# Kernel tuning notes

Measured on AMD Instinct MI355X. Metric: run time of the kernel, lower is better.

## Reference

```python
import jax, jax.numpy as jnp
import numpy as np

N = 100000      # n_nodes
E = 1600000     # n_edges (avg degree 16)
IN_C = 256
OUT_C = 64
HID = OUT_C * 2  # 128


def setup_inputs() -> dict:
    key = jax.random.key(0)
    k = jax.random.split(key, 4)
    x = jax.random.normal(k[0], (N, IN_C), dtype=jnp.float32)
    edge_index = jax.random.randint(k[1], (2, E), 0, N, dtype=jnp.int64)
    W1 = jax.random.normal(k[2], (IN_C, HID), dtype=jnp.float32) * (1.0 / np.sqrt(IN_C))
    b1 = jnp.zeros((HID,), dtype=jnp.float32)
    W2 = jax.random.normal(k[3], (HID, OUT_C), dtype=jnp.float32) * (1.0 / np.sqrt(HID))
    b2 = jnp.zeros((OUT_C,), dtype=jnp.float32)
    return {"x": x, "edge_index": edge_index, "W1": W1, "b1": b1, "W2": W2, "b2": b2}


def reference(x, edge_index, W1, b1, W2, b2):
    n = x.shape[0]
    # GCNConv default: add self-loops, symmetric normalization D^-1/2 A D^-1/2
    loop = jnp.arange(n, dtype=edge_index.dtype)
    src = jnp.concatenate([edge_index[0], loop])  # [E+N]
    dst = jnp.concatenate([edge_index[1], loop])  # [E+N]
    deg = jax.ops.segment_sum(jnp.ones_like(dst, dtype=x.dtype), dst, num_segments=n)
    dis = jax.lax.rsqrt(deg)  # deg >= 1 thanks to self-loops
    norm = dis[src] * dis[dst]  # [E+N]

    def gcn_conv(h, W, b):
        h = h @ W                                   # [n, d_out] dense transform first
        msg = h[src] * norm[:, None]                # [E+N, d_out] gather + scale
        return jax.ops.segment_sum(msg, dst, num_segments=n) + b

    h = jax.nn.relu(gcn_conv(x, W1, b1))
    return gcn_conv(h, W2, b2)
```

## Files before the change

### kernel.cpp

```cpp
#include <hip/hip_runtime.h>
#include <hip/hip_bf16.h>


#define GCN_IN_C 256
#define GCN_HID  128
#define GCN_OUT  64

#define BKT_SHIFT 8
#define BKT_NODES 256
#define EPB 4096

typedef __bf16 bf16x8 __attribute__((ext_vector_type(8)));
typedef __bf16 bf16x4 __attribute__((ext_vector_type(4)));
typedef float f32x4 __attribute__((ext_vector_type(4)));

__global__ __launch_bounds__(256) void k_bucket_hist(const int* __restrict__ dst,
                                                     int* __restrict__ bcnt, int e, int nb) {
  __shared__ int h[512];
  int tid = threadIdx.x;
  h[tid] = 0; h[tid + 256] = 0;
  __syncthreads();
  int base = blockIdx.x * EPB;
#pragma unroll
  for (int j = 0; j < EPB / 256; ++j) {
    int i = base + j * 256 + tid;
    if (i < e) atomicAdd(&h[dst[i] >> BKT_SHIFT], 1);
  }
  __syncthreads();
  if (tid < nb && h[tid]) atomicAdd(&bcnt[tid], h[tid]);
  if (tid + 256 < nb && h[tid + 256]) atomicAdd(&bcnt[tid + 256], h[tid + 256]);
}

__global__ __launch_bounds__(512) void k_scan_buckets(const int* __restrict__ bcnt,
                                                      int* __restrict__ bbase,
                                                      int* __restrict__ bcur, int nb) {
  __shared__ int sh[512];
  int t = threadIdx.x;
  int v = (t < nb) ? bcnt[t] : 0;
  sh[t] = v;
  __syncthreads();
  for (int d = 1; d < 512; d <<= 1) {
    int x = (t >= d) ? sh[t - d] : 0;
    __syncthreads();
    sh[t] += x;
    __syncthreads();
  }
  if (t < nb) {
    int ex = sh[t] - v;
    bbase[t] = ex;
    bcur[t] = ex;
  }
}

__global__ __launch_bounds__(256) void k_partition(const int* __restrict__ src,
                                                   const int* __restrict__ dst,
                                                   int* __restrict__ bcur,
                                                   unsigned int* __restrict__ part,
                                                   int e, int nb) {
  __shared__ int h[512];
  __shared__ int base[512];
  int tid = threadIdx.x;
  h[tid] = 0; h[tid + 256] = 0;
  __syncthreads();
  int b0 = blockIdx.x * EPB;
  int s[EPB / 256], d[EPB / 256], rk[EPB / 256];
#pragma unroll
  for (int j = 0; j < EPB / 256; ++j) {
    int i = b0 + j * 256 + tid;
    if (i < e) {
      s[j] = src[i];
      d[j] = dst[i];
      rk[j] = atomicAdd(&h[d[j] >> BKT_SHIFT], 1);
    }
  }
  __syncthreads();
  if (tid < nb && h[tid]) base[tid] = atomicAdd(&bcur[tid], h[tid]);
  if (tid + 256 < nb && h[tid + 256]) base[tid + 256] = atomicAdd(&bcur[tid + 256], h[tid + 256]);
  __syncthreads();
#pragma unroll
  for (int j = 0; j < EPB / 256; ++j) {
    int i = b0 + j * 256 + tid;
    if (i < e) {
      int bk = d[j] >> BKT_SHIFT;
      unsigned int dl = (unsigned int)(d[j] & (BKT_NODES - 1));
      part[base[bk] + rk[j]] = (dl << 24) | (unsigned int)s[j];
    }
  }
}

__global__ __launch_bounds__(256) void k_bucket_csr(
    const unsigned int* __restrict__ part, const int* __restrict__ bbase,
    const int* __restrict__ bcnt, int* __restrict__ off, int* __restrict__ end,
    float* __restrict__ dis, int* __restrict__ csr, int n) {
  __shared__ int cnt[256];
  __shared__ int sc[256];
  __shared__ int cur[256];
  int b = blockIdx.x, tid = threadIdx.x;
  int node0 = b << BKT_SHIFT;
  int eb0 = bbase[b];
  int ebn = bcnt[b];
  cnt[tid] = 0;
  __syncthreads();
  for (int i = tid; i < ebn; i += 256) atomicAdd(&cnt[part[eb0 + i] >> 24], 1);
  __syncthreads();
  int v = cnt[tid];
  sc[tid] = v;
  __syncthreads();
  for (int dd = 1; dd < 256; dd <<= 1) {
    int x = (tid >= dd) ? sc[tid - dd] : 0;
    __syncthreads();
    sc[tid] += x;
    __syncthreads();
  }
  int lo = sc[tid] - v;
  cur[tid] = lo;
  int node = node0 + tid;
  if (node < n) {
    off[node] = eb0 + lo;
    end[node] = eb0 + lo + v;
    dis[node] = rsqrtf((float)v + 1.0f);
  }
  __syncthreads();
  for (int i = tid; i < ebn; i += 256) {
    unsigned int u = part[eb0 + i];
    int r = atomicAdd(&cur[u >> 24], 1);
    csr[eb0 + r] = (int)(u & 0xFFFFFFu);
  }
}

template<int K, int NOUT>
__device__ __forceinline__ void split_w_one(const float* __restrict__ W,
                                            __bf16* __restrict__ Wsp, int idx) {
  int n = idx % NOUT;
  int g = (idx / NOUT) & 3;
  int ks = idx / (4 * NOUT);
  __bf16* hi = Wsp + (size_t)ks * (2 * 4 * NOUT * 8) + ((size_t)g * NOUT + n) * 8;
  __bf16* lo = hi + 4 * NOUT * 8;
#pragma unroll
  for (int j = 0; j < 8; ++j) {
    float f = W[(size_t)(ks * 32 + g * 8 + j) * NOUT + n];
    __bf16 h = (__bf16)f;
    hi[j] = h;
    lo[j] = (__bf16)(f - (float)h);
  }
}

__global__ __launch_bounds__(256) void k_split_w_all(
    const float* __restrict__ W1, __bf16* __restrict__ w1sp,
    const float* __restrict__ W2, __bf16* __restrict__ w2sp) {
  constexpr int N1 = (GCN_IN_C / 32) * 4 * GCN_HID;
  constexpr int N2 = (GCN_HID / 32) * 4 * GCN_OUT;
  int idx = blockIdx.x * 256 + threadIdx.x;
  if (idx < N1) split_w_one<GCN_IN_C, GCN_HID>(W1, w1sp, idx);
  else if (idx < N1 + N2) split_w_one<GCN_HID, GCN_OUT>(W2, w2sp, idx - N1);
}

template<int K, int NOUT>
__global__ __launch_bounds__(256, 5) void k_gemm_mfma(
    const float* __restrict__ X, const __bf16* __restrict__ Wsp,
    const float* __restrict__ dis, __bf16* __restrict__ T, int M) {
  constexpr int BM = 64;
  constexpr int NF = NOUT / 16;
  constexpr int KSTEPS = K / 32;
  constexpr int TILE = 2 * 4 * NOUT * 8;

  const int tid = threadIdx.x;
  const int wave = tid >> 6;
  const int lane = tid & 63;
  const int l15 = lane & 15;
  const int lg = lane >> 4;
  const int r0w = blockIdx.x * BM + wave * 16;

  f32x4 acc[NF];
#pragma unroll
  for (int nf = 0; nf < NF; ++nf) acc[nf] = (f32x4){0.f, 0.f, 0.f, 0.f};

  int row = r0w + l15;
  int rowA = (row < M) ? row : (M - 1);

  auto loadA = [&](int ks, float4* v0, float4* v1) {
    const float* ap = X + (size_t)rowA * K + ks * 32 + lg * 8;
    *v0 = *(const float4*)ap;
    *v1 = *(const float4*)(ap + 4);
  };

  float4 ca0, ca1, na0, na1;
  loadA(0, &ca0, &ca1);

  const int boff = lg * NOUT * 8 + l15 * 8;
#pragma unroll 1
  for (int ks = 0; ks < KSTEPS; ++ks) {
    if (ks + 1 < KSTEPS) loadA(ks + 1, &na0, &na1);
    bf16x8 ah, al;
    {
      float va[8] = {ca0.x, ca0.y, ca0.z, ca0.w, ca1.x, ca1.y, ca1.z, ca1.w};
#pragma unroll
      for (int j = 0; j < 8; ++j) {
        __bf16 h = (__bf16)va[j];
        ah[j] = h;
        al[j] = (__bf16)(va[j] - (float)h);
      }
    }
    const __bf16* wk = Wsp + (size_t)ks * TILE;
    const __bf16* wkl = wk + 4 * NOUT * 8;
#pragma unroll
    for (int nf = 0; nf < NF; ++nf) {
      bf16x8 bh = *(const bf16x8*)(wk + boff + nf * 128);
      bf16x8 bl = *(const bf16x8*)(wkl + boff + nf * 128);
      acc[nf] = __builtin_amdgcn_mfma_f32_16x16x32_bf16(bh, ah, acc[nf], 0, 0, 0);
      acc[nf] = __builtin_amdgcn_mfma_f32_16x16x32_bf16(bl, ah, acc[nf], 0, 0, 0);
      acc[nf] = __builtin_amdgcn_mfma_f32_16x16x32_bf16(bh, al, acc[nf], 0, 0, 0);
    }
    ca0 = na0;
    ca1 = na1;
  }

  if (row < M) {
    float dv = dis[row];
#pragma unroll
    for (int nf = 0; nf < NF; ++nf) {
      bf16x4 pk;
#pragma unroll
      for (int r = 0; r < 4; ++r) pk[r] = (__bf16)(dv * acc[nf][r]);
      *(bf16x4*)(T + (size_t)row * NOUT + nf * 16 + lg * 4) = pk;
    }
  }
}

template<int K, int NOUT>
__global__ __launch_bounds__(256) void k_gemm_bf16A(
    const __bf16* __restrict__ A, const __bf16* __restrict__ Wsp,
    const float* __restrict__ dis, __bf16* __restrict__ T, int M) {
  constexpr int BM = 64;
  constexpr int NF = NOUT / 16;
  constexpr int KSTEPS = K / 32;
  constexpr int TILE = 2 * 4 * NOUT * 8;

  const int tid = threadIdx.x;
  const int wave = tid >> 6;
  const int lane = tid & 63;
  const int l15 = lane & 15;
  const int lg = lane >> 4;
  const int r0w = blockIdx.x * BM + wave * 16;

  f32x4 acc[NF];
#pragma unroll
  for (int nf = 0; nf < NF; ++nf) acc[nf] = (f32x4){0.f, 0.f, 0.f, 0.f};

  int row = r0w + l15;
  int rowA = (row < M) ? row : (M - 1);

  bf16x8 ca, na;
  ca = *(const bf16x8*)(A + (size_t)rowA * K + lg * 8);

  const int boff = lg * NOUT * 8 + l15 * 8;
#pragma unroll 1
  for (int ks = 0; ks < KSTEPS; ++ks) {
    if (ks + 1 < KSTEPS)
      na = *(const bf16x8*)(A + (size_t)rowA * K + (ks + 1) * 32 + lg * 8);
    const __bf16* wk = Wsp + (size_t)ks * TILE;
    const __bf16* wkl = wk + 4 * NOUT * 8;
#pragma unroll
    for (int nf = 0; nf < NF; ++nf) {
      bf16x8 bh = *(const bf16x8*)(wk + boff + nf * 128);
      bf16x8 bl = *(const bf16x8*)(wkl + boff + nf * 128);
      acc[nf] = __builtin_amdgcn_mfma_f32_16x16x32_bf16(bh, ca, acc[nf], 0, 0, 0);
      acc[nf] = __builtin_amdgcn_mfma_f32_16x16x32_bf16(bl, ca, acc[nf], 0, 0, 0);
    }
    ca = na;
  }

  if (row < M) {
    float dv = dis[row];
#pragma unroll
    for (int nf = 0; nf < NF; ++nf) {
      bf16x4 pk;
#pragma unroll
      for (int r = 0; r < 4; ++r) pk[r] = (__bf16)(dv * acc[nf][r]);
      *(bf16x4*)(T + (size_t)row * NOUT + nf * 16 + lg * 4) = pk;
    }
  }
}

template<int C, bool RELU, typename OutT>
__global__ __launch_bounds__(256) void k_agg_csr(
    const int* __restrict__ csr, const int* __restrict__ off,
    const int* __restrict__ end, const __bf16* __restrict__ ts,
    const float* __restrict__ dis, const float* __restrict__ bias,
    OutT* __restrict__ out, int n) {
  constexpr int LPG = C / 8;
  int gtid = blockIdx.x * 256 + threadIdx.x;
  int node = gtid / LPG;
  int gl = gtid % LPG;
  if (node >= n) return;

  float acc[8];
  {
    bf16x8 v = *(const bf16x8*)(ts + (size_t)node * C + gl * 8);
#pragma unroll
    for (int j = 0; j < 8; ++j) acc[j] = (float)v[j];
  }

  int e = off[node];
  int e1 = end[node];
  for (; e + 4 <= e1; e += 4) {
    int s0 = csr[e];
    int s1 = csr[e + 1];
    int s2 = csr[e + 2];
    int s3 = csr[e + 3];
    bf16x8 v0 = *(const bf16x8*)(ts + (size_t)s0 * C + gl * 8);
    bf16x8 v1 = *(const bf16x8*)(ts + (size_t)s1 * C + gl * 8);
    bf16x8 v2 = *(const bf16x8*)(ts + (size_t)s2 * C + gl * 8);
    bf16x8 v3 = *(const bf16x8*)(ts + (size_t)s3 * C + gl * 8);
#pragma unroll
    for (int j = 0; j < 8; ++j)
      acc[j] += ((float)v0[j] + (float)v1[j]) + ((float)v2[j] + (float)v3[j]);
  }
  for (; e < e1; ++e) {
    int s0 = csr[e];
    bf16x8 v0 = *(const bf16x8*)(ts + (size_t)s0 * C + gl * 8);
#pragma unroll
    for (int j = 0; j < 8; ++j) acc[j] += (float)v0[j];
  }

  float di = dis[node];
  float o[8];
#pragma unroll
  for (int j = 0; j < 8; ++j) {
    o[j] = di * acc[j] + bias[gl * 8 + j];
    if (RELU) o[j] = fmaxf(o[j], 0.f);
  }
  if constexpr (sizeof(OutT) == 2) {
    bf16x8 pv;
#pragma unroll
    for (int j = 0; j < 8; ++j) pv[j] = (__bf16)o[j];
    *(bf16x8*)((__bf16*)out + (size_t)node * C + gl * 8) = pv;
  } else {
    float4* op = (float4*)((float*)out + (size_t)node * C + gl * 8);
    op[0] = make_float4(o[0], o[1], o[2], o[3]);
    op[1] = make_float4(o[4], o[5], o[6], o[7]);
  }
}

extern "C" void kernel_launch(void* const* d_in, const int* in_sizes, int n_in,
                              void* d_out, int out_size, void* d_ws, size_t ws_size,
                              hipStream_t stream) {
  const float* x  = (const float*)d_in[0];
  const int*   ei = (const int*)d_in[1];
  const float* W1 = (const float*)d_in[2];
  const float* b1 = (const float*)d_in[3];
  const float* W2 = (const float*)d_in[4];
  const float* b2 = (const float*)d_in[5];
  float* out = (float*)d_out;

  const int N = in_sizes[0] / GCN_IN_C;
  const int E = in_sizes[1] / 2;
  const int* src = ei;
  const int* dst = ei + E;
  const int NB = (N + BKT_NODES - 1) >> BKT_SHIFT;
  const int EB = (E + EPB - 1) / EPB;

  char* p = (char*)d_ws;
  float* dis = (float*)p;             p += (size_t)N * 4;
  __bf16* t1s = (__bf16*)p;           p += (size_t)N * GCN_HID * 2;
  __bf16* a1  = (__bf16*)p;           p += (size_t)N * GCN_HID * 2;
  int* off   = (int*)p;               p += (size_t)N * 4;
  int* end   = (int*)p;               p += (size_t)N * 4;
  int* csr   = (int*)p;               p += (size_t)E * 4;
  int* bcnt  = (int*)p;               p += 512 * 4;
  int* bbase = (int*)p;               p += 512 * 4;
  int* bcur  = (int*)p;               p += 512 * 4;
  __bf16* w1sp = (__bf16*)p;          p += (size_t)(GCN_IN_C / 32) * 2 * 4 * GCN_HID * 8 * 2;
  __bf16* w2sp = (__bf16*)p;
  unsigned int* part = (unsigned int*)a1;
  __bf16* t2s = t1s;

  k_split_w_all<<<(4096 + 1024 + 255) / 256, 256, 0, stream>>>(W1, w1sp, W2, w2sp);
  hipMemsetAsync(bcnt, 0, 512 * sizeof(int), stream);

  k_bucket_hist<<<EB, 256, 0, stream>>>(dst, bcnt, E, NB);
  k_scan_buckets<<<1, 512, 0, stream>>>(bcnt, bbase, bcur, NB);
  k_partition<<<EB, 256, 0, stream>>>(src, dst, bcur, part, E, NB);
  k_bucket_csr<<<NB, 256, 0, stream>>>(part, bbase, bcnt, off, end, dis, csr, N);

  k_gemm_mfma<GCN_IN_C, GCN_HID>
      <<<(N + 63) / 64, 256, 0, stream>>>(x, w1sp, dis, t1s, N);
  k_agg_csr<GCN_HID, true, __bf16>
      <<<((size_t)N * (GCN_HID / 8) + 255) / 256, 256, 0, stream>>>(csr, off, end, t1s, dis, b1, a1, N);

  k_gemm_bf16A<GCN_HID, GCN_OUT>
      <<<(N + 63) / 64, 256, 0, stream>>>(a1, w2sp, dis, t2s, N);
  k_agg_csr<GCN_OUT, false, float>
      <<<((size_t)N * (GCN_OUT / 8) + 255) / 256, 256, 0, stream>>>(csr, off, end, t2s, dis, b2, out, N);
}
```

Baseline: 218.8 us.

## Process 64 rows per wave in GEMM kernels to reuse weight fragments

Both MFMA GEMM kernels now have each wave compute four 16-row tiles (64 rows) instead of one, so every weight fragment loaded from global memory is reused across four A tiles. Grids shrink fourfold and the launch bounds are relaxed to allow more registers for the larger accumulator arrays. The software prefetch of the next A k-slice is removed, so A loads are no longer overlapped with the MFMAs, and occupancy drops because of the higher register use.

```diff
diff --git a/kernel.cpp b/kernel.cpp
--- a/kernel.cpp
+++ b/kernel.cpp
@@ -156,10 +156,9 @@
 }
 
 template<int K, int NOUT>
-__global__ __launch_bounds__(256, 5) void k_gemm_mfma(
+__global__ __launch_bounds__(256, 2) void k_gemm_mfma(
     const float* __restrict__ X, const __bf16* __restrict__ Wsp,
     const float* __restrict__ dis, __bf16* __restrict__ T, int M) {
-  constexpr int BM = 64;
   constexpr int NF = NOUT / 16;
   constexpr int KSTEPS = K / 32;
   constexpr int TILE = 2 * 4 * NOUT * 8;
@@ -169,36 +168,37 @@
   const int lane = tid & 63;
   const int l15 = lane & 15;
   const int lg = lane >> 4;
-  const int r0w = blockIdx.x * BM + wave * 16;
-
-  f32x4 acc[NF];
-#pragma unroll
-  for (int nf = 0; nf < NF; ++nf) acc[nf] = (f32x4){0.f, 0.f, 0.f, 0.f};
-
-  int row = r0w + l15;
-  int rowA = (row < M) ? row : (M - 1);
-
-  auto loadA = [&](int ks, float4* v0, float4* v1) {
-    const float* ap = X + (size_t)rowA * K + ks * 32 + lg * 8;
-    *v0 = *(const float4*)ap;
-    *v1 = *(const float4*)(ap + 4);
-  };
-
-  float4 ca0, ca1, na0, na1;
-  loadA(0, &ca0, &ca1);
+  const int base = (blockIdx.x * 4 + wave) * 64;
+
+  f32x4 acc[4][NF];
+#pragma unroll
+  for (int t = 0; t < 4; ++t)
+#pragma unroll
+    for (int nf = 0; nf < NF; ++nf) acc[t][nf] = (f32x4){0.f, 0.f, 0.f, 0.f};
+
+  int rowA[4];
+#pragma unroll
+  for (int t = 0; t < 4; ++t) {
+    int r = base + t * 16 + l15;
+    rowA[t] = (r < M) ? r : (M - 1);
+  }
 
   const int boff = lg * NOUT * 8 + l15 * 8;
 #pragma unroll 1
   for (int ks = 0; ks < KSTEPS; ++ks) {
-    if (ks + 1 < KSTEPS) loadA(ks + 1, &na0, &na1);
-    bf16x8 ah, al;
-    {
-      float va[8] = {ca0.x, ca0.y, ca0.z, ca0.w, ca1.x, ca1.y, ca1.z, ca1.w};
+    const int k0 = ks * 32 + lg * 8;
+    bf16x8 ah[4], al[4];
+#pragma unroll
+    for (int t = 0; t < 4; ++t) {
+      const float* ap = X + (size_t)rowA[t] * K + k0;
+      float4 v0 = *(const float4*)ap;
+      float4 v1 = *(const float4*)(ap + 4);
+      float va[8] = {v0.x, v0.y, v0.z, v0.w, v1.x, v1.y, v1.z, v1.w};
 #pragma unroll
       for (int j = 0; j < 8; ++j) {
         __bf16 h = (__bf16)va[j];
-        ah[j] = h;
-        al[j] = (__bf16)(va[j] - (float)h);
+        ah[t][j] = h;
+        al[t][j] = (__bf16)(va[j] - (float)h);
       }
     }
     const __bf16* wk = Wsp + (size_t)ks * TILE;
@@ -207,31 +207,35 @@
     for (int nf = 0; nf < NF; ++nf) {
       bf16x8 bh = *(const bf16x8*)(wk + boff + nf * 128);
       bf16x8 bl = *(const bf16x8*)(wkl + boff + nf * 128);
-      acc[nf] = __builtin_amdgcn_mfma_f32_16x16x32_bf16(bh, ah, acc[nf], 0, 0, 0);
-      acc[nf] = __builtin_amdgcn_mfma_f32_16x16x32_bf16(bl, ah, acc[nf], 0, 0, 0);
-      acc[nf] = __builtin_amdgcn_mfma_f32_16x16x32_bf16(bh, al, acc[nf], 0, 0, 0);
-    }
-    ca0 = na0;
-    ca1 = na1;
-  }
-
-  if (row < M) {
-    float dv = dis[row];
-#pragma unroll
-    for (int nf = 0; nf < NF; ++nf) {
-      bf16x4 pk;
-#pragma unroll
-      for (int r = 0; r < 4; ++r) pk[r] = (__bf16)(dv * acc[nf][r]);
-      *(bf16x4*)(T + (size_t)row * NOUT + nf * 16 + lg * 4) = pk;
+#pragma unroll
+      for (int t = 0; t < 4; ++t) {
+        acc[t][nf] = __builtin_amdgcn_mfma_f32_16x16x32_bf16(bh, ah[t], acc[t][nf], 0, 0, 0);
+        acc[t][nf] = __builtin_amdgcn_mfma_f32_16x16x32_bf16(bl, ah[t], acc[t][nf], 0, 0, 0);
+        acc[t][nf] = __builtin_amdgcn_mfma_f32_16x16x32_bf16(bh, al[t], acc[t][nf], 0, 0, 0);
+      }
+    }
+  }
+
+#pragma unroll
+  for (int t = 0; t < 4; ++t) {
+    int row = base + t * 16 + l15;
+    if (row < M) {
+      float dv = dis[row];
+#pragma unroll
+      for (int nf = 0; nf < NF; ++nf) {
+        bf16x4 pk;
+#pragma unroll
+        for (int r = 0; r < 4; ++r) pk[r] = (__bf16)(dv * acc[t][nf][r]);
+        *(bf16x4*)(T + (size_t)row * NOUT + nf * 16 + lg * 4) = pk;
+      }
     }
   }
 }
 
 template<int K, int NOUT>
-__global__ __launch_bounds__(256) void k_gemm_bf16A(
+__global__ __launch_bounds__(256, 4) void k_gemm_bf16A(
     const __bf16* __restrict__ A, const __bf16* __restrict__ Wsp,
     const float* __restrict__ dis, __bf16* __restrict__ T, int M) {
-  constexpr int BM = 64;
   constexpr int NF = NOUT / 16;
   constexpr int KSTEPS = K / 32;
   constexpr int TILE = 2 * 4 * NOUT * 8;
@@ -241,43 +245,55 @@
   const int lane = tid & 63;
   const int l15 = lane & 15;
   const int lg = lane >> 4;
-  const int r0w = blockIdx.x * BM + wave * 16;
-
-  f32x4 acc[NF];
-#pragma unroll
-  for (int nf = 0; nf < NF; ++nf) acc[nf] = (f32x4){0.f, 0.f, 0.f, 0.f};
-
-  int row = r0w + l15;
-  int rowA = (row < M) ? row : (M - 1);
-
-  bf16x8 ca, na;
-  ca = *(const bf16x8*)(A + (size_t)rowA * K + lg * 8);
+  const int base = (blockIdx.x * 4 + wave) * 64;
+
+  f32x4 acc[4][NF];
+#pragma unroll
+  for (int t = 0; t < 4; ++t)
+#pragma unroll
+    for (int nf = 0; nf < NF; ++nf) acc[t][nf] = (f32x4){0.f, 0.f, 0.f, 0.f};
+
+  int rowA[4];
+#pragma unroll
+  for (int t = 0; t < 4; ++t) {
+    int r = base + t * 16 + l15;
+    rowA[t] = (r < M) ? r : (M - 1);
+  }
 
   const int boff = lg * NOUT * 8 + l15 * 8;
 #pragma unroll 1
   for (int ks = 0; ks < KSTEPS; ++ks) {
-    if (ks + 1 < KSTEPS)
-      na = *(const bf16x8*)(A + (size_t)rowA * K + (ks + 1) * 32 + lg * 8);
+    const int k0 = ks * 32 + lg * 8;
+    bf16x8 ca[4];
+#pragma unroll
+    for (int t = 0; t < 4; ++t)
+      ca[t] = *(const bf16x8*)(A + (size_t)rowA[t] * K + k0);
     const __bf16* wk = Wsp + (size_t)ks * TILE;
     const __bf16* wkl = wk + 4 * NOUT * 8;
 #pragma unroll
     for (int nf = 0; nf < NF; ++nf) {
       bf16x8 bh = *(const bf16x8*)(wk + boff + nf * 128);
       bf16x8 bl = *(const bf16x8*)(wkl + boff + nf * 128);
-      acc[nf] = __builtin_amdgcn_mfma_f32_16x16x32_bf16(bh, ca, acc[nf], 0, 0, 0);
-      acc[nf] = __builtin_amdgcn_mfma_f32_16x16x32_bf16(bl, ca, acc[nf], 0, 0, 0);
-    }
-    ca = na;
-  }
-
-  if (row < M) {
-    float dv = dis[row];
-#pragma unroll
-    for (int nf = 0; nf < NF; ++nf) {
-      bf16x4 pk;
-#pragma unroll
-      for (int r = 0; r < 4; ++r) pk[r] = (__bf16)(dv * acc[nf][r]);
-      *(bf16x4*)(T + (size_t)row * NOUT + nf * 16 + lg * 4) = pk;
+#pragma unroll
+      for (int t = 0; t < 4; ++t) {
+        acc[t][nf] = __builtin_amdgcn_mfma_f32_16x16x32_bf16(bh, ca[t], acc[t][nf], 0, 0, 0);
+        acc[t][nf] = __builtin_amdgcn_mfma_f32_16x16x32_bf16(bl, ca[t], acc[t][nf], 0, 0, 0);
+      }
+    }
+  }
+
+#pragma unroll
+  for (int t = 0; t < 4; ++t) {
+    int row = base + t * 16 + l15;
+    if (row < M) {
+      float dv = dis[row];
+#pragma unroll
+      for (int nf = 0; nf < NF; ++nf) {
+        bf16x4 pk;
+#pragma unroll
+        for (int r = 0; r < 4; ++r) pk[r] = (__bf16)(dv * acc[t][nf][r]);
+        *(bf16x4*)(T + (size_t)row * NOUT + nf * 16 + lg * 4) = pk;
+      }
     }
   }
 }
@@ -384,12 +400,12 @@
   k_bucket_csr<<<NB, 256, 0, stream>>>(part, bbase, bcnt, off, end, dis, csr, N);
 
   k_gemm_mfma<GCN_IN_C, GCN_HID>
-      <<<(N + 63) / 64, 256, 0, stream>>>(x, w1sp, dis, t1s, N);
+      <<<(N + 255) / 256, 256, 0, stream>>>(x, w1sp, dis, t1s, N);
   k_agg_csr<GCN_HID, true, __bf16>
       <<<((size_t)N * (GCN_HID / 8) + 255) / 256, 256, 0, stream>>>(csr, off, end, t1s, dis, b1, a1, N);
 
   k_gemm_bf16A<GCN_HID, GCN_OUT>
-      <<<(N + 63) / 64, 256, 0, stream>>>(a1, w2sp, dis, t2s, N);
+      <<<(N + 255) / 256, 256, 0, stream>>>(a1, w2sp, dis, t2s, N);
   k_agg_csr<GCN_OUT, false, float>
       <<<((size_t)N * (GCN_OUT / 8) + 255) / 256, 256, 0, stream>>>(csr, off, end, t2s, dis, b2, out, N);
 }
```

After: 215.8 us. About the same (-1.4%).
